# Kernel tuning notes

Hardware: AMD Instinct MI355X
Metric: run time of the kernel (lower is better)

Reference implementation:

```python
import jax, jax.numpy as jnp
import numpy as np

N_NODES = 50000
N_EDGES = 800000
D_IN = 64
D_OUT = 64


def setup_inputs() -> dict:
    key = jax.random.key(0)
    k = jax.random.split(key, 5)
    stdv = 1.0 / np.sqrt(D_OUT)
    X = jax.random.normal(k[0], (N_NODES, D_IN), jnp.float32)
    weights = jax.random.uniform(k[1], (D_IN, D_OUT), jnp.float32, -stdv, stdv)
    attention_w = jax.random.normal(k[2], (1, 1), jnp.float32)
    # edge list: row = destination (segment) ids, sorted (CSR-like); col = source ids
    row = jnp.sort(jax.random.randint(k[3], (N_EDGES,), 0, N_NODES, jnp.int32))
    col = jax.random.randint(k[4], (N_EDGES,), 0, N_NODES, jnp.int32)
    return {"X": X, "weights": weights, "attention_w": attention_w, "row": row, "col": col}


def reference(X, weights, attention_w, row, col):
    # dense linear
    Xp = X @ weights  # [N, D_OUT]
    # SDDMM: per-edge dot product between dst and src transformed features
    edge_feature = jnp.einsum('ed,ed->e', Xp[row], Xp[col])  # [E]
    # scale by scalar attention weight (n_heads = 1)
    edge_attn = edge_feature * attention_w[0, 0]  # [E]
    # SpMM aggregation: out[i] = sum_{e: row[e]=i} edge_attn[e] * Xp[col[e]]
    out = jax.ops.segment_sum(edge_attn[:, None] * Xp[col], row,
                              num_segments=X.shape[0])  # [N, D_OUT]
    return out
```

## Files before the change

kernel.cpp:

```cpp
#include <hip/hip_runtime.h>
#include <hip/hip_fp16.h>

#define D 64

__device__ __forceinline__ void h8_to_f32(uint4 u, float f[8]) {
    float2 t;
    t = __half22float2(*(const __half2*)&u.x); f[0] = t.x; f[1] = t.y;
    t = __half22float2(*(const __half2*)&u.y); f[2] = t.x; f[3] = t.y;
    t = __half22float2(*(const __half2*)&u.z); f[4] = t.x; f[5] = t.y;
    t = __half22float2(*(const __half2*)&u.w); f[6] = t.x; f[7] = t.y;
}

__global__ __launch_bounds__(256) void prep_kernel(const float* __restrict__ X,
                                                   const float* __restrict__ W,
                                                   const int* __restrict__ row,
                                                   __half* __restrict__ Xp,
                                                   int* __restrict__ rowptr,
                                                   int nNodes, int nEdges,
                                                   int gemmBlocks) {
    if ((int)blockIdx.x >= gemmBlocks) {
        int e = (blockIdx.x - gemmBlocks) * 256 + threadIdx.x;
        if (e >= nEdges) return;
        int r = row[e];
        int rprev = (e == 0) ? -1 : row[e - 1];
        for (int q = rprev + 1; q <= r; ++q) rowptr[q] = e;
        if (e == nEdges - 1) {
            for (int q = r + 1; q <= nNodes; ++q) rowptr[q] = nEdges;
        }
        return;
    }
    int lane = threadIdx.x & 63;
    int wave = (blockIdx.x * 256 + threadIdx.x) >> 6;
    int nWaves = gemmBlocks * 4;

    float w[D];
#pragma unroll
    for (int k = 0; k < D; ++k) w[k] = W[k * D + lane];

    for (int r = wave; r < nNodes; r += nWaves) {
        int rr = __builtin_amdgcn_readfirstlane(r);
        const float4* xr = (const float4*)(X + (size_t)rr * D);
        float acc = 0.f;
#pragma unroll
        for (int k4 = 0; k4 < D / 4; ++k4) {
            float4 xv = xr[k4];
            acc = fmaf(xv.x, w[4 * k4 + 0], acc);
            acc = fmaf(xv.y, w[4 * k4 + 1], acc);
            acc = fmaf(xv.z, w[4 * k4 + 2], acc);
            acc = fmaf(xv.w, w[4 * k4 + 3], acc);
        }
        Xp[(size_t)rr * D + lane] = __float2half(acc);
    }
}

__global__ __launch_bounds__(256) void fused_kernel(const __half* __restrict__ Xp,
                                                    const int* __restrict__ rowptr,
                                                    const int* __restrict__ col,
                                                    const float* __restrict__ attn_w,
                                                    float* __restrict__ out,
                                                    int nNodes) {
    int lane = threadIdx.x & 63;
    int waveId = (blockIdx.x * 256 + threadIdx.x) >> 6;
    int g = lane >> 3;
    int j = lane & 7;

    int node = waveId * 8 + g;
    bool active = node < nNodes;
    int nd = active ? node : (nNodes - 1);

    int eStart = rowptr[nd];
    int eEnd   = active ? rowptr[nd + 1] : eStart;
    float attn = attn_w[0];

    const uint4* XpV = (const uint4*)Xp;
    float xr[8];
    h8_to_f32(XpV[(size_t)nd * 8 + j], xr);

    float acc[8] = {0.f, 0.f, 0.f, 0.f, 0.f, 0.f, 0.f, 0.f};

    for (int e = eStart; e < eEnd; e += 4) {
        bool v[4];
        int  c[4];
#pragma unroll
        for (int u = 0; u < 4; ++u) {
            int ee = e + u;
            v[u] = ee < eEnd;
            c[u] = col[v[u] ? ee : eStart];
        }
        uint4 raw[4];
#pragma unroll
        for (int u = 0; u < 4; ++u)
            raw[u] = XpV[(size_t)c[u] * 8 + j];

        float xf[4][8];
        float p[4];
#pragma unroll
        for (int u = 0; u < 4; ++u) {
            h8_to_f32(raw[u], xf[u]);
            float s = 0.f;
#pragma unroll
            for (int q = 0; q < 8; ++q) s = fmaf(xr[q], xf[u][q], s);
            p[u] = s;
        }
#pragma unroll
        for (int off = 1; off < 8; off <<= 1) {
#pragma unroll
            for (int u = 0; u < 4; ++u) p[u] += __shfl_xor(p[u], off, 64);
        }
#pragma unroll
        for (int u = 0; u < 4; ++u) {
            float s = v[u] ? p[u] * attn : 0.f;
#pragma unroll
            for (int q = 0; q < 8; ++q) acc[q] = fmaf(s, xf[u][q], acc[q]);
        }
    }

    if (active) {
        float4* o = (float4*)(out + (size_t)node * D + 8 * j);
        o[0] = make_float4(acc[0], acc[1], acc[2], acc[3]);
        o[1] = make_float4(acc[4], acc[5], acc[6], acc[7]);
    }
}

extern "C" void kernel_launch(void* const* d_in, const int* in_sizes, int n_in,
                              void* d_out, int out_size, void* d_ws, size_t ws_size,
                              hipStream_t stream) {
    const float* X    = (const float*)d_in[0];
    const float* W    = (const float*)d_in[1];
    const float* attn = (const float*)d_in[2];
    const int*   row  = (const int*)d_in[3];
    const int*   col  = (const int*)d_in[4];
    float* out = (float*)d_out;

    int nNodes = in_sizes[0] / D;
    int nEdges = in_sizes[3];

    __half* Xp  = (__half*)d_ws;
    int* rowptr = (int*)((char*)d_ws + (size_t)nNodes * D * sizeof(__half));

    int gemmBlocks = 1024;
    int rpBlocks   = (nEdges + 255) / 256;
    prep_kernel<<<gemmBlocks + rpBlocks, 256, 0, stream>>>(X, W, row, Xp, rowptr,
                                                           nNodes, nEdges, gemmBlocks);

    int waves = (nNodes + 7) / 8;
    fused_kernel<<<(waves + 3) / 4, 256, 0, stream>>>(Xp, rowptr, col, attn, out, nNodes);
}
```

Baseline: 106.2 us.

## Software-pipeline neighbor gathers and use packed fp16 dot for SDDMM

The fused kernel now loads the next group of four neighbor rows before computing on the current group, so gather latency overlaps compute. The per-edge dot product uses the fp16 fdot2 builtin on the packed halves instead of converting to fp32 and doing scalar FMAs. The attention scale is applied once at the output store rather than per edge. In exchange the loop holds more registers and issues one extra group of loads past the end of each row.

```diff
diff --git a/kernel.cpp b/kernel.cpp
--- a/kernel.cpp
+++ b/kernel.cpp
@@ -2,6 +2,34 @@
 #include <hip/hip_fp16.h>
 
 #define D 64
+
+typedef _Float16 h16;
+typedef h16 h16x2 __attribute__((ext_vector_type(2)));
+
+__device__ __forceinline__ h16x2 u2h(unsigned int u) {
+    union { unsigned int i; h16x2 h; } t; t.i = u; return t.h;
+}
+
+__device__ __forceinline__ float dot8_f16(uint4 a, uint4 b, float c) {
+#if __has_builtin(__builtin_amdgcn_fdot2)
+    c = __builtin_amdgcn_fdot2(u2h(a.x), u2h(b.x), c, false);
+    c = __builtin_amdgcn_fdot2(u2h(a.y), u2h(b.y), c, false);
+    c = __builtin_amdgcn_fdot2(u2h(a.z), u2h(b.z), c, false);
+    c = __builtin_amdgcn_fdot2(u2h(a.w), u2h(b.w), c, false);
+    return c;
+#else
+    float2 t;
+    t = __half22float2(*(const __half2*)&a.x); float2 s = __half22float2(*(const __half2*)&b.x);
+    c = fmaf(t.x, s.x, c); c = fmaf(t.y, s.y, c);
+    t = __half22float2(*(const __half2*)&a.y); s = __half22float2(*(const __half2*)&b.y);
+    c = fmaf(t.x, s.x, c); c = fmaf(t.y, s.y, c);
+    t = __half22float2(*(const __half2*)&a.z); s = __half22float2(*(const __half2*)&b.z);
+    c = fmaf(t.x, s.x, c); c = fmaf(t.y, s.y, c);
+    t = __half22float2(*(const __half2*)&a.w); s = __half22float2(*(const __half2*)&b.w);
+    c = fmaf(t.x, s.x, c); c = fmaf(t.y, s.y, c);
+    return c;
+#endif
+}
 
 __device__ __forceinline__ void h8_to_f32(uint4 u, float f[8]) {
     float2 t;
@@ -66,59 +94,57 @@
 
     int node = waveId * 8 + g;
     bool active = node < nNodes;
-    int nd = active ? node : (nNodes - 1);
+    int nd = active ? node : 0;
 
     int eStart = rowptr[nd];
     int eEnd   = active ? rowptr[nd + 1] : eStart;
-    float attn = attn_w[0];
 
     const uint4* XpV = (const uint4*)Xp;
-    float xr[8];
-    h8_to_f32(XpV[(size_t)nd * 8 + j], xr);
+    uint4 xr = XpV[(size_t)nd * 8 + j];
 
     float acc[8] = {0.f, 0.f, 0.f, 0.f, 0.f, 0.f, 0.f, 0.f};
 
+    bool v[4]; uint4 raw[4];
+#pragma unroll
+    for (int u = 0; u < 4; ++u) {
+        int ee = eStart + u;
+        v[u] = ee < eEnd;
+        int cc = col[v[u] ? ee : 0];
+        raw[u] = XpV[(size_t)cc * 8 + j];
+    }
+
     for (int e = eStart; e < eEnd; e += 4) {
-        bool v[4];
-        int  c[4];
+        bool v2[4]; uint4 raw2[4];
 #pragma unroll
         for (int u = 0; u < 4; ++u) {
-            int ee = e + u;
-            v[u] = ee < eEnd;
-            c[u] = col[v[u] ? ee : eStart];
+            int ee = e + 4 + u;
+            v2[u] = ee < eEnd;
+            int cc = col[v2[u] ? ee : 0];
+            raw2[u] = XpV[(size_t)cc * 8 + j];
         }
-        uint4 raw[4];
-#pragma unroll
-        for (int u = 0; u < 4; ++u)
-            raw[u] = XpV[(size_t)c[u] * 8 + j];
-
-        float xf[4][8];
         float p[4];
 #pragma unroll
+        for (int u = 0; u < 4; ++u) p[u] = dot8_f16(xr, raw[u], 0.f);
+#pragma unroll
+        for (int off = 1; off < 8; off <<= 1)
+#pragma unroll
+            for (int u = 0; u < 4; ++u) p[u] += __shfl_xor(p[u], off, 64);
+#pragma unroll
         for (int u = 0; u < 4; ++u) {
-            h8_to_f32(raw[u], xf[u]);
-            float s = 0.f;
+            float s = v[u] ? p[u] : 0.f;
+            float xf[8]; h8_to_f32(raw[u], xf);
 #pragma unroll
-            for (int q = 0; q < 8; ++q) s = fmaf(xr[q], xf[u][q], s);
-            p[u] = s;
+            for (int q = 0; q < 8; ++q) acc[q] = fmaf(s, xf[q], acc[q]);
         }
 #pragma unroll
-        for (int off = 1; off < 8; off <<= 1) {
-#pragma unroll
-            for (int u = 0; u < 4; ++u) p[u] += __shfl_xor(p[u], off, 64);
-        }
-#pragma unroll
-        for (int u = 0; u < 4; ++u) {
-            float s = v[u] ? p[u] * attn : 0.f;
-#pragma unroll
-            for (int q = 0; q < 8; ++q) acc[q] = fmaf(s, xf[u][q], acc[q]);
-        }
+        for (int u = 0; u < 4; ++u) { v[u] = v2[u]; raw[u] = raw2[u]; }
     }
 
     if (active) {
+        float attn = attn_w[0];
         float4* o = (float4*)(out + (size_t)node * D + 8 * j);
-        o[0] = make_float4(acc[0], acc[1], acc[2], acc[3]);
-        o[1] = make_float4(acc[4], acc[5], acc[6], acc[7]);
+        o[0] = make_float4(attn * acc[0], attn * acc[1], attn * acc[2], attn * acc[3]);
+        o[1] = make_float4(attn * acc[4], attn * acc[5], attn * acc[6], attn * acc[7]);
     }
 }
 
```

Result: no change. 104.8 us (-1.3%).
